# Kernel optimization log

Hardware: AMD Instinct MI355X
Metric: run time of the kernel (lower is better)

Reference implementation:

```python
import jax, jax.numpy as jnp
import numpy as np
from jax import lax


def _gauss1d(size, sigma):
    k = np.arange(size, dtype=np.float32) - (size - 1) / 2.0
    k = np.exp(-0.5 * (k / sigma) ** 2)
    return k / k.sum()


def _make_kernel(scale, sigma):
    # make_odd
    kx, ky, kz = [s + 1 if s % 2 == 0 else s for s in scale]
    kH = _gauss1d(kx, sigma)
    kW = _gauss1d(ky, sigma)
    kD = _gauss1d(kz, sigma)
    kern = kH[:, None, None] * kW[None, :, None] * kD[None, None, :]  # (kx, ky, kz)
    kern = np.transpose(kern, (2, 0, 1))  # permute(2,0,1) -> (kz, kx, ky)
    return jnp.asarray(kern, dtype=jnp.float32)


def setup_inputs() -> dict:
    key = jax.random.key(0)
    x = jax.random.normal(key, (2, 1, 256, 256, 256), dtype=jnp.float32)
    kernel0 = _make_kernel((2, 2, 2), 1.0)  # (3,3,3)
    kernel1 = _make_kernel((4, 4, 4), 1.0)  # (5,5,5)
    return {"x": x, "kernel0": kernel0, "kernel1": kernel1}


def _blur_down(x, kernel, stride):
    # replicate pad by k//2 per spatial dim, then depthwise (C=1) conv3d.
    pad = [(0, 0), (0, 0)] + [(k // 2, k // 2) for k in kernel.shape]
    xp = jnp.pad(x, pad, mode='edge')
    # strided VALID conv == full blur followed by [::s] slicing (output ceil(H/s))
    return lax.conv_general_dilated(
        xp, kernel[None, None].astype(x.dtype),
        window_strides=stride, padding='VALID',
        dimension_numbers=('NCDHW', 'OIDHW', 'NCDHW'))


def reference(x, kernel0, kernel1):
    d1 = _blur_down(x, kernel0, (2, 2, 2))  # (2,1,128,128,128)
    d2 = _blur_down(x, kernel1, (4, 4, 4))  # (2,1,64,64,64)
    return (x, d1, d2)
```

## Files before the change

### kernel.cpp

```cpp
#include <hip/hip_runtime.h>

#define N_BATCH 2
#define S_IN 256
#define S_D1 128
#define S_D2 64
#define IN_PER_BATCH (S_IN * S_IN * S_IN)
#define D1_PER_BATCH (S_D1 * S_D1 * S_D1)
#define D2_PER_BATCH (S_D2 * S_D2 * S_D2)
#define X_ELEMS (N_BATCH * IN_PER_BATCH)
#define D1_ELEMS (N_BATCH * D1_PER_BATCH)
#define D2_ELEMS (N_BATCH * D2_PER_BATCH)

__global__ __launch_bounds__(256) void d1_kernel(
    const float* __restrict__ x, const float* __restrict__ kern,
    float* __restrict__ out)
{
    __shared__ float kw[27];
    if (threadIdx.x < 27) kw[threadIdx.x] = kern[threadIdx.x];
    __syncthreads();

    int t = blockIdx.x * blockDim.x + threadIdx.x;
    if (t >= D1_ELEMS) return;

    int w = t & (S_D1 - 1);
    int h = (t >> 7) & (S_D1 - 1);
    int d = (t >> 14) & (S_D1 - 1);
    int n = t >> 21;

    const float* xb = x + (size_t)n * IN_PER_BATCH;

    float acc = 0.0f;
#pragma unroll
    for (int a = 0; a < 3; ++a) {
        int iz = 2 * d - 1 + a;
        iz = iz < 0 ? 0 : (iz > S_IN - 1 ? S_IN - 1 : iz);
#pragma unroll
        for (int b = 0; b < 3; ++b) {
            int iy = 2 * h - 1 + b;
            iy = iy < 0 ? 0 : (iy > S_IN - 1 ? S_IN - 1 : iy);
            const float* row = xb + ((size_t)iz * S_IN + iy) * S_IN;
            const float* kr = kw + (a * 3 + b) * 3;
#pragma unroll
            for (int c = 0; c < 3; ++c) {
                int ix = 2 * w - 1 + c;
                ix = ix < 0 ? 0 : (ix > S_IN - 1 ? S_IN - 1 : ix);
                acc = fmaf(kr[c], row[ix], acc);
            }
        }
    }
    out[t] = acc;
}

__global__ __launch_bounds__(256) void d2_kernel(
    const float* __restrict__ x, const float* __restrict__ kern,
    float* __restrict__ out)
{
    __shared__ float kw[125];
    if (threadIdx.x < 125) kw[threadIdx.x] = kern[threadIdx.x];
    __syncthreads();

    int t = blockIdx.x * blockDim.x + threadIdx.x;
    if (t >= D2_ELEMS) return;

    int w = t & (S_D2 - 1);
    int h = (t >> 6) & (S_D2 - 1);
    int d = (t >> 12) & (S_D2 - 1);
    int n = t >> 18;

    const float* xb = x + (size_t)n * IN_PER_BATCH;

    float acc = 0.0f;
#pragma unroll
    for (int a = 0; a < 5; ++a) {
        int iz = 4 * d - 2 + a;
        iz = iz < 0 ? 0 : (iz > S_IN - 1 ? S_IN - 1 : iz);
#pragma unroll
        for (int b = 0; b < 5; ++b) {
            int iy = 4 * h - 2 + b;
            iy = iy < 0 ? 0 : (iy > S_IN - 1 ? S_IN - 1 : iy);
            const float* row = xb + ((size_t)iz * S_IN + iy) * S_IN;
            const float* kr = kw + (a * 5 + b) * 5;
#pragma unroll
            for (int c = 0; c < 5; ++c) {
                int ix = 4 * w - 2 + c;
                ix = ix < 0 ? 0 : (ix > S_IN - 1 ? S_IN - 1 : ix);
                acc = fmaf(kr[c], row[ix], acc);
            }
        }
    }
    out[t] = acc;
}

extern "C" void kernel_launch(void* const* d_in, const int* in_sizes, int n_in,
                              void* d_out, int out_size, void* d_ws, size_t ws_size,
                              hipStream_t stream) {
    const float* x  = (const float*)d_in[0];
    const float* k0 = (const float*)d_in[1];
    const float* k1 = (const float*)d_in[2];

    float* out0 = (float*)d_out;
    float* out1 = out0 + X_ELEMS;
    float* out2 = out1 + D1_ELEMS;

    hipMemcpyAsync(out0, x, (size_t)X_ELEMS * sizeof(float),
                   hipMemcpyDeviceToDevice, stream);

    {
        int threads = 256;
        int blocks = (D1_ELEMS + threads - 1) / threads;
        d1_kernel<<<blocks, threads, 0, stream>>>(x, k0, out1);
    }

    {
        int threads = 256;
        int blocks = (D2_ELEMS + threads - 1) / threads;
        d2_kernel<<<blocks, threads, 0, stream>>>(x, k1, out2);
    }
}
```

Measured before the change: 319.4 us.

## Fuse identity copy and both blur-downsamples into one LDS-tiled kernel

Replaces the device-to-device memcpy and the two separate strided-conv kernels with a single kernel. Each block loads a 20^3 halo tile of x into LDS with edge clamping, writes the 16^3 interior to the identity output, and computes the 8^3 d1 and 4^3 d2 outputs from LDS. The aim is to read x from global memory once instead of three times and to remove two launches. In exchange it uses about 33 KB of LDS per block and rereads a 25% halo, and only 64 threads work on the d2 stage.

```diff
diff --git a/kernel.cpp b/kernel.cpp
--- a/kernel.cpp
+++ b/kernel.cpp
@@ -1,94 +1,101 @@
 #include <hip/hip_runtime.h>
 
-#define N_BATCH 2
 #define S_IN 256
-#define S_D1 128
-#define S_D2 64
-#define IN_PER_BATCH (S_IN * S_IN * S_IN)
-#define D1_PER_BATCH (S_D1 * S_D1 * S_D1)
-#define D2_PER_BATCH (S_D2 * S_D2 * S_D2)
-#define X_ELEMS (N_BATCH * IN_PER_BATCH)
-#define D1_ELEMS (N_BATCH * D1_PER_BATCH)
-#define D2_ELEMS (N_BATCH * D2_PER_BATCH)
+#define IN_PB (S_IN * S_IN * S_IN)
+#define D1_PB (128 * 128 * 128)
+#define D2_PB (64 * 64 * 64)
+#define X_ELEMS (2 * IN_PB)
+#define D1_ELEMS (2 * D1_PB)
 
-__global__ __launch_bounds__(256) void d1_kernel(
-    const float* __restrict__ x, const float* __restrict__ kern,
-    float* __restrict__ out)
+#define T 16
+#define L 20
+#define LROW 21
+#define LSLAB (L * LROW)
+#define LDS_TOT (L * LSLAB)
+
+__global__ __launch_bounds__(256, 4) void pyramid_fused_kernel(
+    const float* __restrict__ x, const float* __restrict__ k0,
+    const float* __restrict__ k1, float* __restrict__ out0,
+    float* __restrict__ out1, float* __restrict__ out2)
 {
-    __shared__ float kw[27];
-    if (threadIdx.x < 27) kw[threadIdx.x] = kern[threadIdx.x];
+    __shared__ float tile[LDS_TOT];
+    __shared__ float kw1[27];
+    __shared__ float kw2[125];
+
+    const int tid = threadIdx.x;
+    const int bx = blockIdx.x;
+    const int by = blockIdx.y;
+    const int bz = blockIdx.z & 15;
+    const int n  = blockIdx.z >> 4;
+
+    if (tid < 27) kw1[tid] = k0[tid];
+    if (tid >= 32 && tid < 157) kw2[tid - 32] = k1[tid - 32];
+
+    const float* xb = x + (size_t)n * IN_PB;
+    const int tx0 = bx * T - 2, ty0 = by * T - 2, tz0 = bz * T - 2;
+
+    for (int i = tid; i < L * L * L; i += 256) {
+        int lx = i % L;
+        int t2 = i / L;
+        int ly = t2 % L;
+        int lz = t2 / L;
+        int gx = min(max(tx0 + lx, 0), S_IN - 1);
+        int gy = min(max(ty0 + ly, 0), S_IN - 1);
+        int gz = min(max(tz0 + lz, 0), S_IN - 1);
+        tile[lz * LSLAB + ly * LROW + lx] =
+            xb[((((size_t)gz << 8) + gy) << 8) + gx];
+    }
     __syncthreads();
 
-    int t = blockIdx.x * blockDim.x + threadIdx.x;
-    if (t >= D1_ELEMS) return;
+    {
+        const size_t ob0 = (size_t)n * IN_PB;
+        for (int i = tid; i < T * T * T; i += 256) {
+            int lx = i & 15, ly = (i >> 4) & 15, lz = i >> 8;
+            float v = tile[(lz + 2) * LSLAB + (ly + 2) * LROW + (lx + 2)];
+            size_t gz = (size_t)(bz * T + lz);
+            out0[ob0 + (((gz << 8) + (by * T + ly)) << 8) + (bx * T + lx)] = v;
+        }
+    }
 
-    int w = t & (S_D1 - 1);
-    int h = (t >> 7) & (S_D1 - 1);
-    int d = (t >> 14) & (S_D1 - 1);
-    int n = t >> 21;
-
-    const float* xb = x + (size_t)n * IN_PER_BATCH;
-
-    float acc = 0.0f;
+    for (int i = tid; i < 8 * 8 * 8; i += 256) {
+        int w = i & 7, h = (i >> 3) & 7, d = i >> 6;
+        float acc = 0.0f;
 #pragma unroll
-    for (int a = 0; a < 3; ++a) {
-        int iz = 2 * d - 1 + a;
-        iz = iz < 0 ? 0 : (iz > S_IN - 1 ? S_IN - 1 : iz);
+        for (int a = 0; a < 3; ++a) {
 #pragma unroll
-        for (int b = 0; b < 3; ++b) {
-            int iy = 2 * h - 1 + b;
-            iy = iy < 0 ? 0 : (iy > S_IN - 1 ? S_IN - 1 : iy);
-            const float* row = xb + ((size_t)iz * S_IN + iy) * S_IN;
-            const float* kr = kw + (a * 3 + b) * 3;
-#pragma unroll
-            for (int c = 0; c < 3; ++c) {
-                int ix = 2 * w - 1 + c;
-                ix = ix < 0 ? 0 : (ix > S_IN - 1 ? S_IN - 1 : ix);
-                acc = fmaf(kr[c], row[ix], acc);
+            for (int b = 0; b < 3; ++b) {
+                const float* r =
+                    &tile[(2 * d + 1 + a) * LSLAB + (2 * h + 1 + b) * LROW + (2 * w + 1)];
+                const float* kr = &kw1[(a * 3 + b) * 3];
+                acc = fmaf(kr[0], r[0], acc);
+                acc = fmaf(kr[1], r[1], acc);
+                acc = fmaf(kr[2], r[2], acc);
             }
         }
+        out1[(size_t)n * D1_PB +
+             (((size_t)(bz * 8 + d) << 7) + (by * 8 + h) << 7) + (bx * 8 + w)] = acc;
     }
-    out[t] = acc;
-}
 
-__global__ __launch_bounds__(256) void d2_kernel(
-    const float* __restrict__ x, const float* __restrict__ kern,
-    float* __restrict__ out)
-{
-    __shared__ float kw[125];
-    if (threadIdx.x < 125) kw[threadIdx.x] = kern[threadIdx.x];
-    __syncthreads();
-
-    int t = blockIdx.x * blockDim.x + threadIdx.x;
-    if (t >= D2_ELEMS) return;
-
-    int w = t & (S_D2 - 1);
-    int h = (t >> 6) & (S_D2 - 1);
-    int d = (t >> 12) & (S_D2 - 1);
-    int n = t >> 18;
-
-    const float* xb = x + (size_t)n * IN_PER_BATCH;
-
-    float acc = 0.0f;
+    if (tid < 64) {
+        int w = tid & 3, h = (tid >> 2) & 3, d = tid >> 4;
+        float acc = 0.0f;
 #pragma unroll
-    for (int a = 0; a < 5; ++a) {
-        int iz = 4 * d - 2 + a;
-        iz = iz < 0 ? 0 : (iz > S_IN - 1 ? S_IN - 1 : iz);
+        for (int a = 0; a < 5; ++a) {
 #pragma unroll
-        for (int b = 0; b < 5; ++b) {
-            int iy = 4 * h - 2 + b;
-            iy = iy < 0 ? 0 : (iy > S_IN - 1 ? S_IN - 1 : iy);
-            const float* row = xb + ((size_t)iz * S_IN + iy) * S_IN;
-            const float* kr = kw + (a * 5 + b) * 5;
-#pragma unroll
-            for (int c = 0; c < 5; ++c) {
-                int ix = 4 * w - 2 + c;
-                ix = ix < 0 ? 0 : (ix > S_IN - 1 ? S_IN - 1 : ix);
-                acc = fmaf(kr[c], row[ix], acc);
+            for (int b = 0; b < 5; ++b) {
+                const float* r =
+                    &tile[(4 * d + a) * LSLAB + (4 * h + b) * LROW + (4 * w)];
+                const float* kr = &kw2[(a * 5 + b) * 5];
+                acc = fmaf(kr[0], r[0], acc);
+                acc = fmaf(kr[1], r[1], acc);
+                acc = fmaf(kr[2], r[2], acc);
+                acc = fmaf(kr[3], r[3], acc);
+                acc = fmaf(kr[4], r[4], acc);
             }
         }
+        out2[(size_t)n * D2_PB +
+             (((size_t)(bz * 4 + d) << 6) + (by * 4 + h) << 6) + (bx * 4 + w)] = acc;
     }
-    out[t] = acc;
 }
 
 extern "C" void kernel_launch(void* const* d_in, const int* in_sizes, int n_in,
@@ -102,18 +109,6 @@
     float* out1 = out0 + X_ELEMS;
     float* out2 = out1 + D1_ELEMS;
 
-    hipMemcpyAsync(out0, x, (size_t)X_ELEMS * sizeof(float),
-                   hipMemcpyDeviceToDevice, stream);
-
-    {
-        int threads = 256;
-        int blocks = (D1_ELEMS + threads - 1) / threads;
-        d1_kernel<<<blocks, threads, 0, stream>>>(x, k0, out1);
-    }
-
-    {
-        int threads = 256;
-        int blocks = (D2_ELEMS + threads - 1) / threads;
-        d2_kernel<<<blocks, threads, 0, stream>>>(x, k1, out2);
-    }
+    dim3 grid(16, 16, 32);
+    pyramid_fused_kernel<<<grid, 256, 0, stream>>>(x, k0, k1, out0, out1, out2);
 }
```

After: 401.9 us. 25.8% more time.
